# Kernel tuning notes

Hardware: AMD Instinct MI355X
Metric: run time of the kernel (lower is better)

The kernel has to match this reference:

```python
import jax, jax.numpy as jnp
import numpy as np

NEG_SLOPE_GAT = 0.2   # PyG GATConv default negative_slope
NEG_SLOPE_ACT = 0.01  # torch F.leaky_relu default


def gat_conv(x, src, dst, W, att_src, att_dst, b, N):
    # Single-head PyG GATConv with self-loops already appended in (src, dst).
    xl = x @ W                              # [N, d]
    a_src = xl @ att_src                    # [N]
    a_dst = xl @ att_dst                    # [N]
    e = jax.nn.leaky_relu(a_src[src] + a_dst[dst], NEG_SLOPE_GAT)  # [E]
    m = jax.ops.segment_max(e, dst, num_segments=N)                # per-dst max
    ex = jnp.exp(e - m[dst])
    s = jax.ops.segment_sum(ex, dst, num_segments=N)
    alpha = ex / (s[dst] + 1e-16)                                  # softmax over in-edges
    out = jax.ops.segment_sum(alpha[:, None] * xl[src], dst, num_segments=N)
    return out + b


def setup_inputs() -> dict:
    key = jax.random.key(0)
    ks = jax.random.split(key, 10)
    N, E, d_in, h1, h2 = 100000, 1600000, 128, 128, 64
    x = jax.random.normal(ks[0], (N, d_in), dtype=jnp.float32)
    edge_index = jax.random.randint(ks[1], (2, E), 0, N, dtype=jnp.int64)
    s1 = 1.0 / np.sqrt(d_in)
    s2 = 1.0 / np.sqrt(h1)
    W1 = jax.random.uniform(ks[2], (d_in, h1), jnp.float32, -s1, s1)
    att_src1 = jax.random.uniform(ks[3], (h1,), jnp.float32, -s2, s2)
    att_dst1 = jax.random.uniform(ks[4], (h1,), jnp.float32, -s2, s2)
    b1 = jnp.zeros((h1,), jnp.float32)
    s3 = 1.0 / np.sqrt(h2)
    W2 = jax.random.uniform(ks[5], (h1, h2), jnp.float32, -s2, s2)
    att_src2 = jax.random.uniform(ks[6], (h2,), jnp.float32, -s3, s3)
    att_dst2 = jax.random.uniform(ks[7], (h2,), jnp.float32, -s3, s3)
    b2 = jnp.zeros((h2,), jnp.float32)
    return {"x": x, "edge_index": edge_index, "W1": W1, "att_src1": att_src1,
            "att_dst1": att_dst1, "b1": b1, "W2": W2, "att_src2": att_src2,
            "att_dst2": att_dst2, "b2": b2}


def reference(x, edge_index, W1, att_src1, att_dst1, b1, W2, att_src2, att_dst2, b2):
    N = x.shape[0]
    loops = jnp.arange(N, dtype=edge_index.dtype)
    src = jnp.concatenate([edge_index[0], loops])  # add self-loops (PyG default)
    dst = jnp.concatenate([edge_index[1], loops])
    h = gat_conv(x, src, dst, W1, att_src1, att_dst1, b1, N)
    h = jax.nn.leaky_relu(h, NEG_SLOPE_ACT)
    # dropout omitted (deterministic reference / eval mode)
    h = gat_conv(h, src, dst, W2, att_src2, att_dst2, b2, N)
    return jax.nn.softmax(h, axis=0)
```

## Files before the change

kernel.cpp:

```cpp
#include <hip/hip_runtime.h>
#include <hip/hip_fp16.h>
#include <math.h>


constexpr int NPARTS = 256;
constexpr int PCAP = 8192;
constexpr int CHUNK = 4096;
constexpr int DPPMAX = 400;

typedef _Float16 f16x8 __attribute__((ext_vector_type(8)));
typedef float f32x4 __attribute__((ext_vector_type(4)));

__device__ __forceinline__ int bcasti(int v, int j) {
  return __builtin_amdgcn_readlane(v, j);
}
__device__ __forceinline__ float bcastf(float v, int j) {
  return __uint_as_float((unsigned)__builtin_amdgcn_readlane((int)__float_as_uint(v), j));
}

__global__ __launch_bounds__(256) void k_build1(
    const int* __restrict__ srcA, const int* __restrict__ dstA,
    int* __restrict__ pcur, uint2* __restrict__ parts,
    int* __restrict__ ovf, int* __restrict__ ovf_cnt,
    const float* __restrict__ W1, const float* __restrict__ W2,
    _Float16* __restrict__ Wf1, _Float16* __restrict__ Wf2,
    int E, int N, int DPP, int nch, int ovfcap) {
  if ((int)blockIdx.x >= nch) {
    int t = ((int)blockIdx.x - nch) * 256 + (int)threadIdx.x;
    const int stride = 8 * 256;
    for (int i = t; i < 8 * 4 * 64 * 8; i += stride) {
      int j = i & 7, l = (i >> 3) & 63, kk = (i >> 9) & 3, cb = i >> 11;
      int k = kk * 32 + (l >> 4) * 8 + j, c = cb * 16 + (l & 15);
      Wf1[i] = (_Float16)W1[k * 128 + c];
    }
    for (int i = t; i < 4 * 4 * 64 * 8; i += stride) {
      int j = i & 7, l = (i >> 3) & 63, kk = (i >> 9) & 3, cb = i >> 11;
      int k = kk * 32 + (l >> 4) * 8 + j, c = cb * 16 + (l & 15);
      Wf2[i] = (_Float16)W2[k * 64 + c];
    }
    return;
  }
  __shared__ int hist[NPARTS];
  __shared__ int base[NPARTS];
  const int tot = E + N;
  const int c = blockIdx.x;
  hist[threadIdx.x] = 0;
  __syncthreads();
  const int beg = c * CHUNK;
  int pp[16], rr[16], ss[16], dd[16];
#pragma unroll
  for (int j = 0; j < 16; ++j) {
    int e = beg + j * 256 + (int)threadIdx.x;
    int d = -1, s = 0;
    if (e < tot) {
      if (e < E) { d = dstA[e]; s = srcA[e]; } else { d = s = e - E; }
    }
    dd[j] = d; ss[j] = s;
    int p = (d >= 0) ? (d / DPP) : -1;
    pp[j] = p;
    rr[j] = (p >= 0) ? atomicAdd(&hist[p], 1) : 0;
  }
  __syncthreads();
  base[threadIdx.x] = atomicAdd(&pcur[threadIdx.x], hist[threadIdx.x]);
  __syncthreads();
#pragma unroll
  for (int j = 0; j < 16; ++j) {
    int p = pp[j];
    if (p < 0) continue;
    int pos = base[p] + rr[j];
    if (pos < PCAP) {
      parts[(size_t)p * PCAP + pos] = make_uint2((unsigned)ss[j], (unsigned)dd[j]);
    } else {
      int o = atomicAdd(ovf_cnt, 1);
      if (o < ovfcap) { ovf[2 * o] = dd[j]; ovf[2 * o + 1] = ss[j]; }
    }
  }
}

template <int C>
__device__ __forceinline__ void gemm_mfma_body(
    const float* __restrict__ X, const _Float16* __restrict__ Wf,
    const float* __restrict__ atts, const float* __restrict__ attd,
    __half* __restrict__ XLh, float* __restrict__ a_s, float* __restrict__ a_d,
    int N, int bid) {
  constexpr int NCB = C / 16;
  const int lane = threadIdx.x & 63;
  const int wv = threadIdx.x >> 6;
  const int r0 = bid * 64 + wv * 16;
  const int arow = lane & 15;
  const int grp = lane >> 4;
  const int r = r0 + arow;
  const int rsafe = (r < N) ? r : (N - 1);

  float av[NCB], dv[NCB];
#pragma unroll
  for (int cb = 0; cb < NCB; ++cb) {
    av[cb] = atts[cb * 16 + arow];
    dv[cb] = attd[cb * 16 + arow];
  }

  f16x8 af[4];
  const float* xr = X + (size_t)rsafe * 128 + grp * 8;
#pragma unroll
  for (int kk = 0; kk < 4; ++kk) {
    float4 u0 = *(const float4*)(xr + kk * 32);
    float4 u1 = *(const float4*)(xr + kk * 32 + 4);
    af[kk][0] = (_Float16)u0.x; af[kk][1] = (_Float16)u0.y;
    af[kk][2] = (_Float16)u0.z; af[kk][3] = (_Float16)u0.w;
    af[kk][4] = (_Float16)u1.x; af[kk][5] = (_Float16)u1.y;
    af[kk][6] = (_Float16)u1.z; af[kk][7] = (_Float16)u1.w;
  }

  float ps[4] = {0.f, 0.f, 0.f, 0.f};
  float pd[4] = {0.f, 0.f, 0.f, 0.f};

#pragma unroll
  for (int cb = 0; cb < NCB; ++cb) {
    f32x4 acc = {0.f, 0.f, 0.f, 0.f};
#pragma unroll
    for (int kk = 0; kk < 4; ++kk) {
      f16x8 bf = *(const f16x8*)(Wf + ((size_t)(cb * 4 + kk) * 64 + lane) * 8);
      acc = __builtin_amdgcn_mfma_f32_16x16x32_f16(af[kk], bf, acc, 0, 0, 0);
    }
    const int ocol = cb * 16 + arow;
#pragma unroll
    for (int i = 0; i < 4; ++i) {
      const int orow = r0 + grp * 4 + i;
      if (orow < N) XLh[(size_t)orow * C + ocol] = (__half)(_Float16)acc[i];
      ps[i] = fmaf(acc[i], av[cb], ps[i]);
      pd[i] = fmaf(acc[i], dv[cb], pd[i]);
    }
  }
#pragma unroll
  for (int m = 1; m < 16; m <<= 1) {
#pragma unroll
    for (int i = 0; i < 4; ++i) {
      ps[i] += __shfl_xor(ps[i], m);
      pd[i] += __shfl_xor(pd[i], m);
    }
  }
  if (arow == 0) {
#pragma unroll
    for (int i = 0; i < 4; ++i) {
      const int orow = r0 + grp * 4 + i;
      if (orow < N) { a_s[orow] = ps[i]; a_d[orow] = pd[i]; }
    }
  }
}

struct PlaceSmem {
  int sc[NPARTS];
  int l_cnt[DPPMAX];
  int l_off[DPPMAX];
  int l_out[PCAP];
};

__global__ __launch_bounds__(256) void k_gemm1_place(
    const float* __restrict__ X, const _Float16* __restrict__ Wf,
    const float* __restrict__ atts, const float* __restrict__ attd,
    __half* __restrict__ XLh, float* __restrict__ a_s, float* __restrict__ a_d,
    int N, const uint2* __restrict__ parts, const int* __restrict__ pcur,
    int* __restrict__ rowptr, int* __restrict__ seidx,
    int DPP, int nparts, int gb) {
  __shared__ PlaceSmem sm;
  if ((int)blockIdx.x < gb) {
    gemm_mfma_body<128>(X, Wf, atts, attd, XLh, a_s, a_d, N, blockIdx.x);
    return;
  }
  const int p = (int)blockIdx.x - gb;
  const int t = threadIdx.x;
  sm.sc[t] = min(pcur[t], PCAP);
  __syncthreads();
  for (int o = 1; o < NPARTS; o <<= 1) {
    int x = (t >= o) ? sm.sc[t - o] : 0;
    __syncthreads();
    sm.sc[t] += x;
    __syncthreads();
  }
  const int base = (p == 0) ? 0 : sm.sc[p - 1];
  const int n = sm.sc[p] - base;
  const int d0 = p * DPP;
  const int ndst = min(DPP, N - d0);
  const uint2* pe = parts + (size_t)p * PCAP;

  for (int i = t; i < ndst; i += 256) sm.l_cnt[i] = 0;
  __syncthreads();
  for (int i = t; i < n; i += 256) {
    uint2 e = pe[i];
    atomicAdd(&sm.l_cnt[(int)e.y - d0], 1);
  }
  __syncthreads();
  if (t == 0) {
    int run = 0;
    for (int i = 0; i < ndst; ++i) { sm.l_off[i] = run; run += sm.l_cnt[i]; }
  }
  __syncthreads();
  for (int i = t; i < ndst; i += 256) {
    rowptr[d0 + i] = base + sm.l_off[i];
    sm.l_cnt[i] = sm.l_off[i];
  }
  if (p == nparts - 1 && t == 0) rowptr[N] = sm.sc[nparts - 1];
  __syncthreads();
  for (int i = t; i < n; i += 256) {
    uint2 e = pe[i];
    int pos = atomicAdd(&sm.l_cnt[(int)e.y - d0], 1);
    sm.l_out[pos] = (int)e.x;
  }
  __syncthreads();
  for (int i = t; i < n; i += 256)
    seidx[base + i] = sm.l_out[i];
}

__global__ __launch_bounds__(256) void k_gemm_l2(
    const float* __restrict__ X, const _Float16* __restrict__ Wf,
    const float* __restrict__ atts, const float* __restrict__ attd,
    __half* __restrict__ XLh, float* __restrict__ a_s, float* __restrict__ a_d,
    int N) {
  gemm_mfma_body<64>(X, Wf, atts, attd, XLh, a_s, a_d, N, blockIdx.x);
}

__global__ __launch_bounds__(256) void k_aggr_l1(
    const __half* __restrict__ XLh, const float* __restrict__ as_,
    const float* __restrict__ ad_, const int* __restrict__ rowptr,
    const int* __restrict__ seidx, const int* __restrict__ ovf,
    const int* __restrict__ ovf_cnt, const float* __restrict__ bias,
    float* __restrict__ OUT, int N) {
  constexpr int C = 128;
  const int lane = threadIdx.x & 63;
  const int wid = threadIdx.x >> 6;
  const int novf = *ovf_cnt;
  const float bb0 = bias[lane * 2], bb1 = bias[lane * 2 + 1];

  for (int d = blockIdx.x * 4 + wid; d < N; d += gridDim.x * 4) {
    const int beg = rowptr[d], end = rowptr[d + 1];
    const int nb = end - beg;
    const float adst = ad_[d];

    float s;
    int sv = 0; float ev = 0.f;
    if (nb <= 64) {
      if (lane < nb) {
        sv = seidx[beg + lane];
        float t = as_[sv] + adst;
        t = t > 0.f ? t : 0.2f * t;
        ev = __expf(t);
      }
      s = ev;
    } else {
      s = 0.f;
      for (int i = beg + lane; i < end; i += 64) {
        int s2 = seidx[i];
        float t = as_[s2] + adst;
        t = t > 0.f ? t : 0.2f * t;
        s += __expf(t);
      }
    }
#pragma unroll
    for (int o = 32; o; o >>= 1) s += __shfl_xor(s, o);

    if (novf > 0) {
      float so = 0.f;
      for (int i = lane; i < novf; i += 64) {
        if (ovf[2 * i] == d) {
          float t = as_[ovf[2 * i + 1]] + adst;
          t = t > 0.f ? t : 0.2f * t;
          so += __expf(t);
        }
      }
#pragma unroll
      for (int o = 32; o; o >>= 1) so += __shfl_xor(so, o);
      s += so;
    }
    const float inv = 1.f / (s + 1e-16f);

    float2 acc = make_float2(0.f, 0.f);
    if (nb <= 64) {
      const float wv = ev * inv;
      auto body = [&](int j) {
        int sj = bcasti(sv, j);
        float wj = bcastf(wv, j);
        const __half2* rp = (const __half2*)(XLh + (size_t)sj * C) + lane;
        float2 xv = __half22float2(*rp);
        acc.x = fmaf(wj, xv.x, acc.x);
        acc.y = fmaf(wj, xv.y, acc.y);
      };
      int j = 0;
      for (; j + 4 <= nb; j += 4) { body(j); body(j + 1); body(j + 2); body(j + 3); }
      for (; j < nb; ++j) body(j);
    } else {
      for (int i0 = beg; i0 < end; i0 += 64) {
        const int nc = min(64, end - i0);
        int sc = 0; float wc = 0.f;
        if (lane < nc) {
          sc = seidx[i0 + lane];
          float t = as_[sc] + adst;
          t = t > 0.f ? t : 0.2f * t;
          wc = __expf(t) * inv;
        }
        for (int j = 0; j < nc; ++j) {
          int sj = bcasti(sc, j);
          float wj = bcastf(wc, j);
          const __half2* rp = (const __half2*)(XLh + (size_t)sj * C) + lane;
          float2 xv = __half22float2(*rp);
          acc.x = fmaf(wj, xv.x, acc.x);
          acc.y = fmaf(wj, xv.y, acc.y);
        }
      }
    }

    if (novf > 0) {
      for (int i = 0; i < novf; ++i) {
        if (ovf[2 * i] != d) continue;
        int os = ovf[2 * i + 1];
        float t = as_[os] + adst;
        t = t > 0.f ? t : 0.2f * t;
        float wj = __expf(t) * inv;
        const __half2* rp = (const __half2*)(XLh + (size_t)os * C) + lane;
        float2 xv = __half22float2(*rp);
        acc.x = fmaf(wj, xv.x, acc.x);
        acc.y = fmaf(wj, xv.y, acc.y);
      }
    }

    float o0 = acc.x + bb0;
    float o1 = acc.y + bb1;
    o0 = o0 > 0.f ? o0 : 0.01f * o0;
    o1 = o1 > 0.f ? o1 : 0.01f * o1;
    *(float2*)&OUT[(size_t)d * C + lane * 2] = make_float2(o0, o1);
  }
}

__global__ __launch_bounds__(256) void k_aggr2(
    const __half* __restrict__ XLh, const float* __restrict__ as_,
    const float* __restrict__ ad_, const int* __restrict__ rowptr,
    const int* __restrict__ seidx, const int* __restrict__ ovf,
    const int* __restrict__ ovf_cnt, const float* __restrict__ bias,
    float* __restrict__ OUT, float* __restrict__ csum8, int N) {
  constexpr int C = 64;
  const int lane = threadIdx.x & 63;
  const int wid = threadIdx.x >> 6;
  const int novf = *ovf_cnt;
  const float bb = bias[lane];
  float cs = 0.f;

  for (int d = blockIdx.x * 4 + wid; d < N; d += gridDim.x * 4) {
    const int beg = rowptr[d], end = rowptr[d + 1];
    const int nb = end - beg;
    const float adst = ad_[d];

    float s;
    int sv = 0; float ev = 0.f;
    if (nb <= 64) {
      if (lane < nb) {
        sv = seidx[beg + lane];
        float t = as_[sv] + adst;
        t = t > 0.f ? t : 0.2f * t;
        ev = __expf(t);
      }
      s = ev;
    } else {
      s = 0.f;
      for (int i = beg + lane; i < end; i += 64) {
        int s2 = seidx[i];
        float t = as_[s2] + adst;
        t = t > 0.f ? t : 0.2f * t;
        s += __expf(t);
      }
    }
#pragma unroll
    for (int o = 32; o; o >>= 1) s += __shfl_xor(s, o);

    if (novf > 0) {
      float so = 0.f;
      for (int i = lane; i < novf; i += 64) {
        if (ovf[2 * i] == d) {
          float t = as_[ovf[2 * i + 1]] + adst;
          t = t > 0.f ? t : 0.2f * t;
          so += __expf(t);
        }
      }
#pragma unroll
      for (int o = 32; o; o >>= 1) so += __shfl_xor(so, o);
      s += so;
    }
    const float inv = 1.f / (s + 1e-16f);

    float acc0 = 0.f;
    if (nb <= 64) {
      const float wv = ev * inv;
      auto body = [&](int j) {
        int sj = bcasti(sv, j);
        float wj = bcastf(wv, j);
        acc0 = fmaf(wj, __half2float(XLh[(size_t)sj * C + lane]), acc0);
      };
      int j = 0;
      for (; j + 4 <= nb; j += 4) { body(j); body(j + 1); body(j + 2); body(j + 3); }
      for (; j < nb; ++j) body(j);
    } else {
      for (int i0 = beg; i0 < end; i0 += 64) {
        const int nc = min(64, end - i0);
        int sc = 0; float wc = 0.f;
        if (lane < nc) {
          sc = seidx[i0 + lane];
          float t = as_[sc] + adst;
          t = t > 0.f ? t : 0.2f * t;
          wc = __expf(t) * inv;
        }
        for (int j = 0; j < nc; ++j) {
          int sj = bcasti(sc, j);
          float wj = bcastf(wc, j);
          acc0 = fmaf(wj, __half2float(XLh[(size_t)sj * C + lane]), acc0);
        }
      }
    }

    if (novf > 0) {
      for (int i = 0; i < novf; ++i) {
        if (ovf[2 * i] != d) continue;
        int os = ovf[2 * i + 1];
        float t = as_[os] + adst;
        t = t > 0.f ? t : 0.2f * t;
        float wj = __expf(t) * inv;
        acc0 = fmaf(wj, __half2float(XLh[(size_t)os * C + lane]), acc0);
      }
    }

    float o0 = acc0 + bb;
    OUT[(size_t)d * C + lane] = o0;
    cs += __expf(o0);
  }

  __shared__ float csA[4][64];
  csA[wid][lane] = cs;
  __syncthreads();
  if (threadIdx.x < 64) {
    float tot = csA[0][threadIdx.x] + csA[1][threadIdx.x] +
                csA[2][threadIdx.x] + csA[3][threadIdx.x];
    if (tot != 0.f)
      atomicAdd(&csum8[((int)blockIdx.x & 7) * 64 + (int)threadIdx.x], tot);
  }
}

__global__ void k_norm(float* __restrict__ O, const float* __restrict__ csum8,
                       size_t tot4) {
  __shared__ float cs[64];
  if (threadIdx.x < 64) {
    float s = 0.f;
#pragma unroll
    for (int r = 0; r < 8; ++r) s += csum8[r * 64 + (int)threadIdx.x];
    cs[threadIdx.x] = s;
  }
  __syncthreads();
  for (size_t i = blockIdx.x * (size_t)blockDim.x + threadIdx.x; i < tot4;
       i += (size_t)gridDim.x * blockDim.x) {
    float4 v = ((float4*)O)[i];
    int c0 = (int)((i * 4) & 63);
    v.x = __expf(v.x) / cs[c0];
    v.y = __expf(v.y) / cs[c0 + 1];
    v.z = __expf(v.z) / cs[c0 + 2];
    v.w = __expf(v.w) / cs[c0 + 3];
    ((float4*)O)[i] = v;
  }
}

extern "C" void kernel_launch(void* const* d_in, const int* in_sizes, int n_in,
                              void* d_out, int out_size, void* d_ws, size_t ws_size,
                              hipStream_t stream) {
  const float* x   = (const float*)d_in[0];
  const int*   ei  = (const int*)d_in[1];
  const float* W1  = (const float*)d_in[2];
  const float* as1 = (const float*)d_in[3];
  const float* ad1 = (const float*)d_in[4];
  const float* b1  = (const float*)d_in[5];
  const float* W2  = (const float*)d_in[6];
  const float* as2 = (const float*)d_in[7];
  const float* ad2 = (const float*)d_in[8];
  const float* b2  = (const float*)d_in[9];
  float* out = (float*)d_out;

  const int N = in_sizes[0] / 128;
  const int E = in_sizes[1] / 2;
  const int Etot = E + N;
  const int* srcA = ei;
  const int* dstA = ei + E;
  const int DPP = (N + NPARTS - 1) / NPARTS;
  const int nparts = (N + DPP - 1) / DPP;

  char* w = (char*)d_ws;
  auto take = [&](size_t bytes) -> void* {
    void* p = (void*)w;
    w += (bytes + 255) & ~(size_t)255;
    return p;
  };
  __half*    xlh   = (__half*)take((size_t)N * 128 * 2);
  __half*    xl2h  = (__half*)take((size_t)N * 64 * 2);
  float*     h     = (float*)take((size_t)N * 128 * 4);
  float*     a_s   = (float*)take((size_t)N * 4);
  float*     a_d   = (float*)take((size_t)N * 4);
  int*       zeroB = (int*)take((size_t)(1 + NPARTS + 512) * 4);
  int*       ovf_cnt = zeroB;
  int*       pcur    = zeroB + 1;
  float*     csum8   = (float*)(zeroB + 1 + NPARTS);
  int*       rowptr = (int*)take((size_t)(N + 1) * 4);
  int*       seidx  = (int*)take((size_t)Etot * 4);
  int*       ovf    = (int*)take((size_t)Etot * 2 * 4);
  uint2*     parts  = (uint2*)take((size_t)NPARTS * PCAP * 8);
  _Float16*  wf1    = (_Float16*)take((size_t)8 * 4 * 64 * 8 * 2);
  _Float16*  wf2    = (_Float16*)take((size_t)4 * 4 * 64 * 8 * 2);

  hipMemsetAsync(zeroB, 0, (size_t)(1 + NPARTS + 512) * 4, stream);

  const int nch = (Etot + CHUNK - 1) / CHUNK;
  const int gb = (N + 63) / 64;

  k_build1<<<nch + 8, 256, 0, stream>>>(srcA, dstA, pcur, parts, ovf, ovf_cnt,
                                        W1, W2, wf1, wf2, E, N, DPP, nch, Etot);
  k_gemm1_place<<<gb + NPARTS, 256, 0, stream>>>(
      x, wf1, as1, ad1, xlh, a_s, a_d, N, parts, pcur, rowptr, seidx,
      DPP, nparts, gb);
  k_aggr_l1<<<8192, 256, 0, stream>>>(xlh, a_s, a_d, rowptr, seidx, ovf, ovf_cnt,
                                      b1, h, N);
  k_gemm_l2<<<gb, 256, 0, stream>>>(h, wf2, as2, ad2, xl2h, a_s, a_d, N);
  k_aggr2<<<8192, 256, 0, stream>>>(xl2h, a_s, a_d, rowptr, seidx, ovf, ovf_cnt,
                                    b2, out, csum8, N);
  const size_t tot4 = (size_t)N * 64 / 4;
  k_norm<<<2048, 256, 0, stream>>>(out, csum8, tot4);
}
```

Measured before the change: 234.8 us.

## Store layer-1 activations in fp16 and gather two edges per wavefront in aggregation

The intermediate activation h between the two GAT layers is now stored as fp16 instead of fp32, and the layer-2 GEMM reads it directly as f16x8 vectors, which halves that write and read traffic. Both aggregation kernels also split each wave into two half-waves, each gathering a different neighbor row with wider per-lane loads. The two halves are combined with a cross-half shuffle, so the number of serial gather iterations per destination is halved. In exchange, h is rounded to fp16 (the GEMM already cast it to fp16, so little changes there), and odd-degree nodes leave half the wave idle on the last step.

```diff
diff --git a/kernel.cpp b/kernel.cpp
--- a/kernel.cpp
+++ b/kernel.cpp
@@ -77,9 +77,9 @@
   }
 }
 
-template <int C>
+template <int C, typename XT>
 __device__ __forceinline__ void gemm_mfma_body(
-    const float* __restrict__ X, const _Float16* __restrict__ Wf,
+    const XT* __restrict__ X, const _Float16* __restrict__ Wf,
     const float* __restrict__ atts, const float* __restrict__ attd,
     __half* __restrict__ XLh, float* __restrict__ a_s, float* __restrict__ a_d,
     int N, int bid) {
@@ -100,15 +100,22 @@
   }
 
   f16x8 af[4];
-  const float* xr = X + (size_t)rsafe * 128 + grp * 8;
-#pragma unroll
-  for (int kk = 0; kk < 4; ++kk) {
-    float4 u0 = *(const float4*)(xr + kk * 32);
-    float4 u1 = *(const float4*)(xr + kk * 32 + 4);
-    af[kk][0] = (_Float16)u0.x; af[kk][1] = (_Float16)u0.y;
-    af[kk][2] = (_Float16)u0.z; af[kk][3] = (_Float16)u0.w;
-    af[kk][4] = (_Float16)u1.x; af[kk][5] = (_Float16)u1.y;
-    af[kk][6] = (_Float16)u1.z; af[kk][7] = (_Float16)u1.w;
+  if constexpr (sizeof(XT) == 4) {
+    const float* xr = (const float*)X + (size_t)rsafe * 128 + grp * 8;
+#pragma unroll
+    for (int kk = 0; kk < 4; ++kk) {
+      float4 u0 = *(const float4*)(xr + kk * 32);
+      float4 u1 = *(const float4*)(xr + kk * 32 + 4);
+      af[kk][0] = (_Float16)u0.x; af[kk][1] = (_Float16)u0.y;
+      af[kk][2] = (_Float16)u0.z; af[kk][3] = (_Float16)u0.w;
+      af[kk][4] = (_Float16)u1.x; af[kk][5] = (_Float16)u1.y;
+      af[kk][6] = (_Float16)u1.z; af[kk][7] = (_Float16)u1.w;
+    }
+  } else {
+    const __half* xr = (const __half*)X + (size_t)rsafe * 128 + grp * 8;
+#pragma unroll
+    for (int kk = 0; kk < 4; ++kk)
+      af[kk] = *(const f16x8*)(xr + kk * 32);
   }
 
   float ps[4] = {0.f, 0.f, 0.f, 0.f};
@@ -164,7 +171,7 @@
     int DPP, int nparts, int gb) {
   __shared__ PlaceSmem sm;
   if ((int)blockIdx.x < gb) {
-    gemm_mfma_body<128>(X, Wf, atts, attd, XLh, a_s, a_d, N, blockIdx.x);
+    gemm_mfma_body<128, float>(X, Wf, atts, attd, XLh, a_s, a_d, N, blockIdx.x);
     return;
   }
   const int p = (int)blockIdx.x - gb;
@@ -212,11 +219,11 @@
 }
 
 __global__ __launch_bounds__(256) void k_gemm_l2(
-    const float* __restrict__ X, const _Float16* __restrict__ Wf,
+    const __half* __restrict__ X, const _Float16* __restrict__ Wf,
     const float* __restrict__ atts, const float* __restrict__ attd,
     __half* __restrict__ XLh, float* __restrict__ a_s, float* __restrict__ a_d,
     int N) {
-  gemm_mfma_body<64>(X, Wf, atts, attd, XLh, a_s, a_d, N, blockIdx.x);
+  gemm_mfma_body<64, __half>(X, Wf, atts, attd, XLh, a_s, a_d, N, blockIdx.x);
 }
 
 __global__ __launch_bounds__(256) void k_aggr_l1(
@@ -224,12 +231,16 @@
     const float* __restrict__ ad_, const int* __restrict__ rowptr,
     const int* __restrict__ seidx, const int* __restrict__ ovf,
     const int* __restrict__ ovf_cnt, const float* __restrict__ bias,
-    float* __restrict__ OUT, int N) {
+    __half* __restrict__ OUT, int N) {
   constexpr int C = 128;
   const int lane = threadIdx.x & 63;
   const int wid = threadIdx.x >> 6;
+  const int grp = lane >> 5;
+  const int l5 = lane & 31;
   const int novf = *ovf_cnt;
-  const float bb0 = bias[lane * 2], bb1 = bias[lane * 2 + 1];
+  float bb[4];
+#pragma unroll
+  for (int j = 0; j < 4; ++j) bb[j] = bias[4 * l5 + j];
 
   for (int d = blockIdx.x * 4 + wid; d < N; d += gridDim.x * 4) {
     const int beg = rowptr[d], end = rowptr[d + 1];
@@ -273,20 +284,33 @@
     }
     const float inv = 1.f / (s + 1e-16f);
 
-    float2 acc = make_float2(0.f, 0.f);
+    float a0 = 0.f, a1 = 0.f, a2 = 0.f, a3 = 0.f;
+    auto pair = [&](int vsrc, float vw, int j, int cnt) {
+      const int j0 = 2 * j, j1 = 2 * j + 1;
+      const int s0 = bcasti(vsrc, j0);
+      const float w0 = bcastf(vw, j0);
+      int s1 = s0; float w1 = 0.f;
+      if (j1 < cnt) { s1 = bcasti(vsrc, j1); w1 = bcastf(vw, j1); }
+      const int sb = grp ? s1 : s0;
+      const float wj = grp ? w1 : w0;
+      const float2 raw = *(const float2*)(XLh + (size_t)sb * C + l5 * 4);
+      float2 x0 = __half22float2(*(const __half2*)&raw.x);
+      float2 x1 = __half22float2(*(const __half2*)&raw.y);
+      a0 = fmaf(wj, x0.x, a0);
+      a1 = fmaf(wj, x0.y, a1);
+      a2 = fmaf(wj, x1.x, a2);
+      a3 = fmaf(wj, x1.y, a3);
+    };
+
     if (nb <= 64) {
       const float wv = ev * inv;
-      auto body = [&](int j) {
-        int sj = bcasti(sv, j);
-        float wj = bcastf(wv, j);
-        const __half2* rp = (const __half2*)(XLh + (size_t)sj * C) + lane;
-        float2 xv = __half22float2(*rp);
-        acc.x = fmaf(wj, xv.x, acc.x);
-        acc.y = fmaf(wj, xv.y, acc.y);
-      };
+      const int np = (nb + 1) >> 1;
       int j = 0;
-      for (; j + 4 <= nb; j += 4) { body(j); body(j + 1); body(j + 2); body(j + 3); }
-      for (; j < nb; ++j) body(j);
+      for (; j + 4 <= np; j += 4) {
+        pair(sv, wv, j, nb); pair(sv, wv, j + 1, nb);
+        pair(sv, wv, j + 2, nb); pair(sv, wv, j + 3, nb);
+      }
+      for (; j < np; ++j) pair(sv, wv, j, nb);
     } else {
       for (int i0 = beg; i0 < end; i0 += 64) {
         const int nc = min(64, end - i0);
@@ -297,16 +321,15 @@
           t = t > 0.f ? t : 0.2f * t;
           wc = __expf(t) * inv;
         }
-        for (int j = 0; j < nc; ++j) {
-          int sj = bcasti(sc, j);
-          float wj = bcastf(wc, j);
-          const __half2* rp = (const __half2*)(XLh + (size_t)sj * C) + lane;
-          float2 xv = __half22float2(*rp);
-          acc.x = fmaf(wj, xv.x, acc.x);
-          acc.y = fmaf(wj, xv.y, acc.y);
-        }
-      }
-    }
+        const int np = (nc + 1) >> 1;
+        for (int j = 0; j < np; ++j) pair(sc, wc, j, nc);
+      }
+    }
+
+    a0 += __shfl_xor(a0, 32);
+    a1 += __shfl_xor(a1, 32);
+    a2 += __shfl_xor(a2, 32);
+    a3 += __shfl_xor(a3, 32);
 
     if (novf > 0) {
       for (int i = 0; i < novf; ++i) {
@@ -315,18 +338,30 @@
         float t = as_[os] + adst;
         t = t > 0.f ? t : 0.2f * t;
         float wj = __expf(t) * inv;
-        const __half2* rp = (const __half2*)(XLh + (size_t)os * C) + lane;
-        float2 xv = __half22float2(*rp);
-        acc.x = fmaf(wj, xv.x, acc.x);
-        acc.y = fmaf(wj, xv.y, acc.y);
-      }
-    }
-
-    float o0 = acc.x + bb0;
-    float o1 = acc.y + bb1;
-    o0 = o0 > 0.f ? o0 : 0.01f * o0;
-    o1 = o1 > 0.f ? o1 : 0.01f * o1;
-    *(float2*)&OUT[(size_t)d * C + lane * 2] = make_float2(o0, o1);
+        const float2 raw = *(const float2*)(XLh + (size_t)os * C + l5 * 4);
+        float2 x0 = __half22float2(*(const __half2*)&raw.x);
+        float2 x1 = __half22float2(*(const __half2*)&raw.y);
+        a0 = fmaf(wj, x0.x, a0);
+        a1 = fmaf(wj, x0.y, a1);
+        a2 = fmaf(wj, x1.x, a2);
+        a3 = fmaf(wj, x1.y, a3);
+      }
+    }
+
+    if (grp == 0) {
+      float o0 = a0 + bb[0], o1 = a1 + bb[1];
+      float o2 = a2 + bb[2], o3 = a3 + bb[3];
+      o0 = o0 > 0.f ? o0 : 0.01f * o0;
+      o1 = o1 > 0.f ? o1 : 0.01f * o1;
+      o2 = o2 > 0.f ? o2 : 0.01f * o2;
+      o3 = o3 > 0.f ? o3 : 0.01f * o3;
+      __half2 p0 = __floats2half2_rn(o0, o1);
+      __half2 p1 = __floats2half2_rn(o2, o3);
+      uint2 u;
+      u.x = *(unsigned*)&p0;
+      u.y = *(unsigned*)&p1;
+      *(uint2*)(OUT + (size_t)d * C + l5 * 4) = u;
+    }
   }
 }
 
@@ -339,9 +374,11 @@
   constexpr int C = 64;
   const int lane = threadIdx.x & 63;
   const int wid = threadIdx.x >> 6;
+  const int grp = lane >> 5;
+  const int l5 = lane & 31;
   const int novf = *ovf_cnt;
-  const float bb = bias[lane];
-  float cs = 0.f;
+  const float bb0 = bias[2 * l5], bb1 = bias[2 * l5 + 1];
+  float cs0 = 0.f, cs1 = 0.f;
 
   for (int d = blockIdx.x * 4 + wid; d < N; d += gridDim.x * 4) {
     const int beg = rowptr[d], end = rowptr[d + 1];
@@ -385,17 +422,30 @@
     }
     const float inv = 1.f / (s + 1e-16f);
 
-    float acc0 = 0.f;
+    float a0 = 0.f, a1 = 0.f;
+    auto pair = [&](int vsrc, float vw, int j, int cnt) {
+      const int j0 = 2 * j, j1 = 2 * j + 1;
+      const int s0 = bcasti(vsrc, j0);
+      const float w0 = bcastf(vw, j0);
+      int s1 = s0; float w1 = 0.f;
+      if (j1 < cnt) { s1 = bcasti(vsrc, j1); w1 = bcastf(vw, j1); }
+      const int sb = grp ? s1 : s0;
+      const float wj = grp ? w1 : w0;
+      const __half2 hv = *(const __half2*)(XLh + (size_t)sb * C + l5 * 2);
+      float2 xv = __half22float2(hv);
+      a0 = fmaf(wj, xv.x, a0);
+      a1 = fmaf(wj, xv.y, a1);
+    };
+
     if (nb <= 64) {
       const float wv = ev * inv;
-      auto body = [&](int j) {
-        int sj = bcasti(sv, j);
-        float wj = bcastf(wv, j);
-        acc0 = fmaf(wj, __half2float(XLh[(size_t)sj * C + lane]), acc0);
-      };
+      const int np = (nb + 1) >> 1;
       int j = 0;
-      for (; j + 4 <= nb; j += 4) { body(j); body(j + 1); body(j + 2); body(j + 3); }
-      for (; j < nb; ++j) body(j);
+      for (; j + 4 <= np; j += 4) {
+        pair(sv, wv, j, nb); pair(sv, wv, j + 1, nb);
+        pair(sv, wv, j + 2, nb); pair(sv, wv, j + 3, nb);
+      }
+      for (; j < np; ++j) pair(sv, wv, j, nb);
     } else {
       for (int i0 = beg; i0 < end; i0 += 64) {
         const int nc = min(64, end - i0);
@@ -406,13 +456,13 @@
           t = t > 0.f ? t : 0.2f * t;
           wc = __expf(t) * inv;
         }
-        for (int j = 0; j < nc; ++j) {
-          int sj = bcasti(sc, j);
-          float wj = bcastf(wc, j);
-          acc0 = fmaf(wj, __half2float(XLh[(size_t)sj * C + lane]), acc0);
-        }
-      }
-    }
+        const int np = (nc + 1) >> 1;
+        for (int j = 0; j < np; ++j) pair(sc, wc, j, nc);
+      }
+    }
+
+    a0 += __shfl_xor(a0, 32);
+    a1 += __shfl_xor(a1, 32);
 
     if (novf > 0) {
       for (int i = 0; i < novf; ++i) {
@@ -421,17 +471,24 @@
         float t = as_[os] + adst;
         t = t > 0.f ? t : 0.2f * t;
         float wj = __expf(t) * inv;
-        acc0 = fmaf(wj, __half2float(XLh[(size_t)os * C + lane]), acc0);
-      }
-    }
-
-    float o0 = acc0 + bb;
-    OUT[(size_t)d * C + lane] = o0;
-    cs += __expf(o0);
+        const __half2 hv = *(const __half2*)(XLh + (size_t)os * C + l5 * 2);
+        float2 xv = __half22float2(hv);
+        a0 = fmaf(wj, xv.x, a0);
+        a1 = fmaf(wj, xv.y, a1);
+      }
+    }
+
+    if (grp == 0) {
+      float o0 = a0 + bb0;
+      float o1 = a1 + bb1;
+      *(float2*)&OUT[(size_t)d * C + 2 * l5] = make_float2(o0, o1);
+      cs0 += __expf(o0);
+      cs1 += __expf(o1);
+    }
   }
 
   __shared__ float csA[4][64];
-  csA[wid][lane] = cs;
+  if (grp == 0) { csA[wid][2 * l5] = cs0; csA[wid][2 * l5 + 1] = cs1; }
   __syncthreads();
   if (threadIdx.x < 64) {
     float tot = csA[0][threadIdx.x] + csA[1][threadIdx.x] +
@@ -494,7 +551,7 @@
   };
   __half*    xlh   = (__half*)take((size_t)N * 128 * 2);
   __half*    xl2h  = (__half*)take((size_t)N * 64 * 2);
-  float*     h     = (float*)take((size_t)N * 128 * 4);
+  __half*    h     = (__half*)take((size_t)N * 128 * 2);
   float*     a_s   = (float*)take((size_t)N * 4);
   float*     a_d   = (float*)take((size_t)N * 4);
   int*       zeroB = (int*)take((size_t)(1 + NPARTS + 512) * 4);
```

Result: faster. 225.3 us (-4.1%).
